# Optimization experiments

Measured on AMD Instinct MI355X. Metric: run time of the kernel, lower is better.

Reference implementation:

```python
import jax, jax.numpy as jnp
import numpy as np

N, E = 100000, 1600000
D_IN, D_HID, D_OUT = 128, 64, 64
NEG_SLOPE = 0.2


def setup_inputs() -> dict:
    key = jax.random.key(0)
    ks = jax.random.split(key, 12)
    x = jax.random.normal(ks[0], (N, D_IN), dtype=jnp.float32)
    edge_index = jax.random.randint(ks[1], (2, E), 0, N, dtype=jnp.int64)
    edge_attr = jax.random.normal(ks[2], (E, 8), dtype=jnp.float32)
    s1 = 1.0 / np.sqrt(D_IN)
    s2 = 1.0 / np.sqrt(D_HID)
    return {
        "x": x,
        "edge_index": edge_index,
        "edge_attr": edge_attr,
        "W1": jax.random.normal(ks[3], (D_IN, D_HID), dtype=jnp.float32) * s1,
        "att_src1": jax.random.normal(ks[4], (D_HID,), dtype=jnp.float32) * s2,
        "att_dst1": jax.random.normal(ks[5], (D_HID,), dtype=jnp.float32) * s2,
        "b1": jnp.zeros((D_HID,), dtype=jnp.float32),
        "W2": jax.random.normal(ks[6], (D_HID, D_OUT), dtype=jnp.float32) * s2,
        "att_src2": jax.random.normal(ks[7], (D_OUT,), dtype=jnp.float32) * (1.0 / np.sqrt(D_OUT)),
        "att_dst2": jax.random.normal(ks[8], (D_OUT,), dtype=jnp.float32) * (1.0 / np.sqrt(D_OUT)),
        "b2": jnp.zeros((D_OUT,), dtype=jnp.float32),
    }


def gat_conv(x, src, dst, W, att_src, att_dst, b, n_nodes):
    # h = W x  (single head)
    h = x @ W                                   # [N, F]
    a_src = h @ att_src                         # [N]
    a_dst = h @ att_dst                         # [N]
    e = jax.nn.leaky_relu(a_src[src] + a_dst[dst], NEG_SLOPE)  # [E]
    # softmax over incoming edges per target node (numerically stable)
    e_max = jax.ops.segment_max(e, dst, num_segments=n_nodes)
    w = jnp.exp(e - e_max[dst])
    denom = jax.ops.segment_sum(w, dst, num_segments=n_nodes)
    alpha = w / (denom[dst] + 1e-16)            # [E]
    out = jax.ops.segment_sum(h[src] * alpha[:, None], dst, num_segments=n_nodes)
    return out + b


def reference(x, edge_index, edge_attr, W1, att_src1, att_dst1, b1, W2, att_src2, att_dst2, b2):
    n_nodes = x.shape[0]
    # PyG GATConv default: add self-loops; edge_attr unused (edge_dim=None)
    loops = jnp.arange(n_nodes, dtype=edge_index.dtype)
    src = jnp.concatenate([edge_index[0], loops])
    dst = jnp.concatenate([edge_index[1], loops])
    h = gat_conv(x, src, dst, W1, att_src1, att_dst1, b1, n_nodes)
    h = jax.nn.relu(h)
    h = gat_conv(h, src, dst, W2, att_src2, att_dst2, b2, n_nodes)
    # global_mean_pool with batch=None -> mean over all nodes, shape [1, D_OUT]
    return jnp.mean(h, axis=0, keepdims=True)
```

## Files before the change

kernel.cpp:

```cpp
#include <hip/hip_runtime.h>
#include <hip/hip_bf16.h>
#include <cstdint>

#define NEG_SLOPE 0.2f
#define BUCKET_SHIFT 9
#define CHUNK 4096

typedef __attribute__((ext_vector_type(4))) int            i32x4;
typedef __attribute__((ext_vector_type(4))) float          f32x4;
typedef __attribute__((ext_vector_type(8))) unsigned short u16x8;
typedef __attribute__((ext_vector_type(4))) unsigned short u16x4;

__device__ inline unsigned short f2bf(float f) {
    unsigned xi = __float_as_uint(f);
    unsigned r = xi + 0x7fffu + ((xi >> 16) & 1u);
    return (unsigned short)(r >> 16);
}
__device__ inline float bflo(unsigned g) { return __uint_as_float(g << 16); }
__device__ inline float bfhi(unsigned g) { return __uint_as_float(g & 0xffff0000u); }

__device__ inline int get_ei(const int* ei, int is64, long idx) {
    return is64 ? ei[2 * idx] : ei[(int)idx];
}

__device__ inline int detect_is64(const int* __restrict__ ei, int tid) {
    __shared__ int dred[4];
    int v = 0;
    for (int i = tid; i < 2048; i += 256) v |= ei[2 * i + 1];
#pragma unroll
    for (int off = 32; off; off >>= 1) v |= __shfl_xor(v, off);
    if ((tid & 63) == 0) dred[tid >> 6] = v;
    __syncthreads();
    int r = dred[0] | dred[1] | dred[2] | dred[3];
    __syncthreads();
    return (r == 0) ? 1 : 0;
}

__device__ void p1_body(const int* __restrict__ ei, int* __restrict__ BT,
                        int E, int n, int bid) {
    __shared__ int cnt[256];
    int tid = threadIdx.x;
    int is64 = detect_is64(ei, tid);
    int nbuk = (n + 511) >> BUCKET_SHIFT;
    for (int b = tid; b < nbuk; b += 256) cnt[b] = 0;
    __syncthreads();
    int total = E + n;
    int beg = bid * CHUNK;
    int end = beg + CHUNK; if (end > total) end = total;
    for (int i = beg + tid; i < end; i += 256) {
        int d = (i < E) ? get_ei(ei, is64, (long)E + i) : (i - E);
        atomicAdd(&cnt[d >> BUCKET_SHIFT], 1);
    }
    __syncthreads();
    for (int b = tid; b < nbuk; b += 256)
        if (cnt[b]) atomicAdd(&BT[b], cnt[b]);
}

#define MFMA_BF16(acc, a, b) \
    asm("s_nop 1\n\tv_mfma_f32_16x16x32_bf16 %0, %1, %2, %0" \
        : "+v"(acc) : "v"(a), "v"(b))

template <int KT, bool XBF>
__device__ void proj_body(const void* __restrict__ xin,
                          const unsigned short* __restrict__ Wp,
                          const float* __restrict__ att_s,
                          const float* __restrict__ att_d,
                          unsigned short* __restrict__ h2,
                          float* __restrict__ asrc,
                          float* __restrict__ adst, int n, int bid) {
    constexpr int K = 32 * KT;
    __shared__ alignas(16) unsigned short lb[4][16 * 72];
    int tid = threadIdx.x;
    int wid = tid >> 6, l = tid & 63;
    int lm = l & 15, lg = l >> 4;

    int node0 = bid * 64 + wid * 16;
    if (node0 >= n) return;

    float as_c[4], ad_c[4];
#pragma unroll
    for (int ct = 0; ct < 4; ++ct) {
        as_c[ct] = att_s[16 * ct + lm];
        ad_c[ct] = att_d[16 * ct + lm];
    }

    f32x4 acc[4] = {};
    int arow = node0 + lm;
    bool rowok = arow < n;

#pragma unroll
    for (int kt = 0; kt < KT; ++kt) {
        i32x4 af = {0, 0, 0, 0};
        if (XBF) {
            const unsigned short* xb = (const unsigned short*)xin
                                       + (size_t)arow * K + 32 * kt + 8 * lg;
            if (rowok) af = *(const i32x4*)xb;
        } else {
            const float* xp = (const float*)xin + (size_t)arow * K + 8 * lg + 32 * kt;
            float4 v0 = make_float4(0.f, 0.f, 0.f, 0.f);
            float4 v1 = v0;
            if (rowok) {
                v0 = *(const float4*)(xp);
                v1 = *(const float4*)(xp + 4);
            }
            af[0] = (int)((unsigned)f2bf(v0.x) | ((unsigned)f2bf(v0.y) << 16));
            af[1] = (int)((unsigned)f2bf(v0.z) | ((unsigned)f2bf(v0.w) << 16));
            af[2] = (int)((unsigned)f2bf(v1.x) | ((unsigned)f2bf(v1.y) << 16));
            af[3] = (int)((unsigned)f2bf(v1.z) | ((unsigned)f2bf(v1.w) << 16));
        }
#pragma unroll
        for (int ct = 0; ct < 4; ++ct) {
            i32x4 bf = *(const i32x4*)(Wp + (((kt * 4 + ct) * 64) + l) * 8);
            MFMA_BF16(acc[ct], af, bf);
        }
    }
    asm volatile("s_nop 7\n\ts_nop 7"
                 : "+v"(acc[0]), "+v"(acc[1]), "+v"(acc[2]), "+v"(acc[3]));

    float ps[4], pd[4];
#pragma unroll
    for (int r = 0; r < 4; ++r) {
        float s = 0.f, d = 0.f;
#pragma unroll
        for (int ct = 0; ct < 4; ++ct) {
            s = fmaf(acc[ct][r], as_c[ct], s);
            d = fmaf(acc[ct][r], ad_c[ct], d);
        }
        ps[r] = s; pd[r] = d;
    }
#pragma unroll
    for (int off = 1; off < 16; off <<= 1) {
#pragma unroll
        for (int r = 0; r < 4; ++r) {
            ps[r] += __shfl_xor(ps[r], off);
            pd[r] += __shfl_xor(pd[r], off);
        }
    }
    if (lm == 0) {
#pragma unroll
        for (int r = 0; r < 4; ++r) {
            int node = node0 + 4 * lg + r;
            if (node < n) { asrc[node] = ps[r]; adst[node] = pd[r]; }
        }
    }

    unsigned short* wb = lb[wid];
#pragma unroll
    for (int ct = 0; ct < 4; ++ct)
#pragma unroll
        for (int r = 0; r < 4; ++r)
            wb[(4 * lg + r) * 72 + 16 * ct + lm] = f2bf(acc[ct][r]);
    asm volatile("s_waitcnt lgkmcnt(0)" ::: "memory");
    int ch = l & 7;
#pragma unroll
    for (int p = 0; p < 2; ++p) {
        int rr = (l >> 3) + 8 * p;
        u16x8 ov = *(const u16x8*)(wb + rr * 72 + 8 * ch);
        int onode = node0 + rr;
        if (onode < n)
            *(u16x8*)(h2 + (size_t)onode * 64 + 8 * ch) = ov;
    }
}

__global__ __launch_bounds__(256) void prep_kernel(const float* __restrict__ W1,
                                                   const float* __restrict__ W2,
                                                   unsigned short* __restrict__ wp1,
                                                   unsigned short* __restrict__ wp2,
                                                   int* __restrict__ BT, int nbuk) {
    if (blockIdx.x == 6) {
        for (int b = threadIdx.x; b < nbuk; b += 256) BT[b] = 0;
        return;
    }
    int t = blockIdx.x * 256 + threadIdx.x;
    int f = t >> 6, l = t & 63;
    int lm = l & 15, lg = l >> 4;
    const float* W = (f < 16) ? W1 : W2;
    unsigned short* wp = (f < 16) ? wp1 : wp2;
    int idx = (f < 16) ? f : (f - 16);
    int kt = idx >> 2, ct = idx & 3;
    union { u16x8 v; unsigned short u[8]; } o;
#pragma unroll
    for (int e = 0; e < 8; ++e)
        o.u[e] = f2bf(W[(size_t)(32 * kt + 8 * lg + e) * 64 + 16 * ct + lm]);
    *(u16x8*)(wp + ((size_t)idx * 64 + l) * 8) = o.v;
}

__global__ __launch_bounds__(256) void fused1(const float* __restrict__ x,
                                              const unsigned short* __restrict__ wp1,
                                              const float* __restrict__ as1,
                                              const float* __restrict__ ad1,
                                              unsigned short* __restrict__ h2,
                                              float* __restrict__ asrc,
                                              float* __restrict__ adst, int n,
                                              const int* __restrict__ ei,
                                              int* __restrict__ BT, int E, int pgrid) {
    if ((int)blockIdx.x < pgrid)
        proj_body<4, false>(x, wp1, as1, ad1, h2, asrc, adst, n, blockIdx.x);
    else
        p1_body(ei, BT, E, n, blockIdx.x - pgrid);
}

__global__ __launch_bounds__(256) void scan_bt(const int* __restrict__ BT,
                                               int* __restrict__ BB,
                                               int* __restrict__ cur, int nbuk) {
    __shared__ int s[256];
    int t = threadIdx.x;
    int v = (t < nbuk) ? BT[t] : 0;
    s[t] = v;
    __syncthreads();
    for (int off = 1; off < 256; off <<= 1) {
        int u = (t >= off) ? s[t - off] : 0;
        __syncthreads();
        s[t] += u;
        __syncthreads();
    }
    int exc = s[t] - v;
    if (t < nbuk) { BB[t] = exc; cur[t] = exc; }
    if (t == 0) BB[nbuk] = s[255];
}

__global__ __launch_bounds__(256) void p3_scatter(const int* __restrict__ ei,
                                                  int* __restrict__ cur,
                                                  int* __restrict__ sorted,
                                                  int E, int n) {
    __shared__ int stash[CHUNK];
    __shared__ unsigned char stashB[CHUNK];
    __shared__ int cnt[256];
    __shared__ int base[256];
    int tid = threadIdx.x;
    int is64 = detect_is64(ei, tid);
    int nbuk = (n + 511) >> BUCKET_SHIFT;
    for (int b = tid; b < nbuk; b += 256) cnt[b] = 0;
    __syncthreads();
    int total = E + n;
    int beg = blockIdx.x * CHUNK;
    int end = beg + CHUNK; if (end > total) end = total;
    for (int i = beg + tid; i < end; i += 256) {
        int s, d;
        if (i < E) {
            s = get_ei(ei, is64, i);
            d = get_ei(ei, is64, (long)E + i);
        } else {
            s = d = i - E;
        }
        int li = i - beg;
        stash[li] = (s << BUCKET_SHIFT) | (d & 511);
        stashB[li] = (unsigned char)(d >> BUCKET_SHIFT);
        atomicAdd(&cnt[d >> BUCKET_SHIFT], 1);
    }
    __syncthreads();
    for (int b = tid; b < nbuk; b += 256) {
        int c = cnt[b];
        base[b] = c ? atomicAdd(&cur[b], c) : 0;
        cnt[b] = 0;
    }
    __syncthreads();
    int cc = end - beg;
    for (int li = tid; li < cc; li += 256) {
        int b = stashB[li];
        int p = base[b] + atomicAdd(&cnt[b], 1);
        sorted[p] = stash[li];
    }
}

__global__ __launch_bounds__(256) void p4_finalize(const int* __restrict__ BB,
                                                   const int* __restrict__ sorted,
                                                   int* __restrict__ ptr,
                                                   int* __restrict__ csr_src,
                                                   int n, int T) {
    int b = blockIdx.x;
    int tid = threadIdx.x;
    int node0 = b << BUCKET_SHIFT;
    int nn = n - node0; if (nn > 512) nn = 512;
    int beg = BB[b];
    int end = BB[b + 1];

    __shared__ int cnt[512];
    __shared__ int pair[256];
    __shared__ int exc[512];
    cnt[tid] = 0; cnt[tid + 256] = 0;
    __syncthreads();
    for (int j = beg + tid; j < end; j += 256) {
        int v = sorted[j];
        atomicAdd(&cnt[v & 511], 1);
    }
    __syncthreads();
    int psum = cnt[2 * tid] + cnt[2 * tid + 1];
    pair[tid] = psum;
    __syncthreads();
    for (int off = 1; off < 256; off <<= 1) {
        int u = (tid >= off) ? pair[tid - off] : 0;
        __syncthreads();
        pair[tid] += u;
        __syncthreads();
    }
    int pexc = pair[tid] - psum;
    exc[2 * tid] = pexc;
    exc[2 * tid + 1] = pexc + cnt[2 * tid];
    __syncthreads();
    for (int i = tid; i < nn; i += 256) ptr[node0 + i] = beg + exc[i];
    if (node0 + nn == n && tid == 0) ptr[n] = T;
    cnt[tid] = exc[tid]; cnt[tid + 256] = exc[tid + 256];
    __syncthreads();
    for (int j = beg + tid; j < end; j += 256) {
        int v = sorted[j];
        int p = beg + atomicAdd(&cnt[v & 511], 1);
        csr_src[p] = ((unsigned)v) >> BUCKET_SHIFT;
    }
}

__global__ __launch_bounds__(256) void proj2_kernel(const unsigned short* __restrict__ xin,
                                                    const unsigned short* __restrict__ wp2,
                                                    const float* __restrict__ as2,
                                                    const float* __restrict__ ad2,
                                                    unsigned short* __restrict__ h2,
                                                    float* __restrict__ asrc,
                                                    float* __restrict__ adst, int n) {
    proj_body<2, true>(xin, wp2, as2, ad2, h2, asrc, adst, n, blockIdx.x);
}

template <bool FMEAN>
__global__ __launch_bounds__(256) void agg_kernel(const int* __restrict__ ptr,
                                                  const int* __restrict__ srcs,
                                                  const unsigned short* __restrict__ h2,
                                                  const float* __restrict__ asrc,
                                                  const float* __restrict__ adst,
                                                  const float* __restrict__ bias,
                                                  unsigned short* __restrict__ outbf,
                                                  float* __restrict__ partials,
                                                  int n, int do_relu) {
    __shared__ int2  sm[4][64];
    __shared__ float red[256];
    int tid = threadIdx.x;
    int lane = tid & 63, wid = tid >> 6;
    int slot = lane >> 4, f = lane & 15;
    const char* h2b = (const char*)h2;
    unsigned fo = (unsigned)f << 3;
    float4 bv = *(const float4*)(bias + 4 * f);
    float ms0 = 0.f, ms1 = 0.f, ms2 = 0.f, ms3 = 0.f;

    int gwave = (blockIdx.x * blockDim.x + tid) >> 6;
    int nwaves = (gridDim.x * blockDim.x) >> 6;
    for (int node = gwave; node < n; node += nwaves) {
        int beg = ptr[node], end = ptr[node + 1];
        float ad = adst[node];
        float a0 = 0.f, a1 = 0.f, a2 = 0.f, a3 = 0.f, wsum = 0.f;
        for (int b = beg; b < end; b += 64) {
            int blen = end - b; if (blen > 64) blen = 64;
            int sv = 0; float wv = 0.f;
            if (lane < blen) {
                sv = srcs[b + lane];
                float e = asrc[sv] + ad;
                e = (e > 0.f) ? e : NEG_SLOPE * e;
                wv = __expf(e);
            }
            wsum += wv;
            sm[wid][lane] = make_int2(sv, __float_as_int(wv));
            int ni = (blen + 15) >> 4;
            for (int j = 0; j < ni; ++j) {
                int2 swv[4];
#pragma unroll
                for (int u = 0; u < 4; ++u)
                    swv[u] = sm[wid][16 * j + 4 * u + slot];
                uint2 g[4]; float w[4];
#pragma unroll
                for (int u = 0; u < 4; ++u) {
                    w[u] = __int_as_float(swv[u].y);
                    g[u] = *(const uint2*)(h2b + (((unsigned)swv[u].x << 7) + fo));
                }
#pragma unroll
                for (int u = 0; u < 4; ++u) {
                    a0 = fmaf(w[u], bflo(g[u].x), a0);
                    a1 = fmaf(w[u], bfhi(g[u].x), a1);
                    a2 = fmaf(w[u], bflo(g[u].y), a2);
                    a3 = fmaf(w[u], bfhi(g[u].y), a3);
                }
            }
        }
        a0 += __shfl_xor(a0, 16); a0 += __shfl_xor(a0, 32);
        a1 += __shfl_xor(a1, 16); a1 += __shfl_xor(a1, 32);
        a2 += __shfl_xor(a2, 16); a2 += __shfl_xor(a2, 32);
        a3 += __shfl_xor(a3, 16); a3 += __shfl_xor(a3, 32);
#pragma unroll
        for (int off = 32; off; off >>= 1) wsum += __shfl_xor(wsum, off);
        float inv = 1.f / (wsum + 1e-16f);
        float o0 = a0 * inv + bv.x;
        float o1 = a1 * inv + bv.y;
        float o2 = a2 * inv + bv.z;
        float o3 = a3 * inv + bv.w;
        if (!FMEAN) {
            if (do_relu) {
                o0 = fmaxf(o0, 0.f); o1 = fmaxf(o1, 0.f);
                o2 = fmaxf(o2, 0.f); o3 = fmaxf(o3, 0.f);
            }
            if (slot == 0) {
                u16x4 ov;
                ov[0] = f2bf(o0); ov[1] = f2bf(o1);
                ov[2] = f2bf(o2); ov[3] = f2bf(o3);
                *(u16x4*)(outbf + (size_t)node * 64 + 4 * f) = ov;
            }
        } else {
            if (slot == 0) { ms0 += o0; ms1 += o1; ms2 += o2; ms3 += o3; }
        }
    }
    if (FMEAN) {
        if (slot == 0)
            *(float4*)(red + wid * 64 + 4 * f) = make_float4(ms0, ms1, ms2, ms3);
        __syncthreads();
        if (tid < 64) {
            float t = red[tid] + red[64 + tid] + red[128 + tid] + red[192 + tid];
            partials[(size_t)blockIdx.x * 64 + tid] = t;
        }
    }
}

__global__ __launch_bounds__(256) void reduce1(const float* __restrict__ partials,
                                               float* __restrict__ out256, int nb) {
    __shared__ float red[256];
    int f = threadIdx.x & 63;
    int w = threadIdx.x >> 6;
    float s = 0.f;
    for (int r = blockIdx.x + 256 * w; r < nb; r += 1024)
        s += partials[(size_t)r * 64 + f];
    red[threadIdx.x] = s;
    __syncthreads();
    if (w == 0) {
        float t = red[f] + red[64 + f] + red[128 + f] + red[192 + f];
        out256[(size_t)blockIdx.x * 64 + f] = t;
    }
}

__global__ __launch_bounds__(1024) void reduce2(const float* __restrict__ out256,
                                                float* __restrict__ out, float inv_n) {
    __shared__ float red[1024];
    int f = threadIdx.x & 63;
    int w = threadIdx.x >> 6;
    float s = 0.f;
    for (int r = w; r < 256; r += 16) s += out256[(size_t)r * 64 + f];
    red[threadIdx.x] = s;
    __syncthreads();
    for (int step = 8; step >= 1; step >>= 1) {
        if (w < step) red[w * 64 + f] += red[(w + step) * 64 + f];
        __syncthreads();
    }
    if (w == 0) out[f] = red[f] * inv_n;
}

extern "C" void kernel_launch(void* const* d_in, const int* in_sizes, int n_in,
                              void* d_out, int out_size, void* d_ws, size_t ws_size,
                              hipStream_t stream) {
    const float* x   = (const float*)d_in[0];
    const int*   ei  = (const int*)d_in[1];
    const float* W1  = (const float*)d_in[3];
    const float* as1 = (const float*)d_in[4];
    const float* ad1 = (const float*)d_in[5];
    const float* b1  = (const float*)d_in[6];
    const float* W2  = (const float*)d_in[7];
    const float* as2 = (const float*)d_in[8];
    const float* ad2 = (const float*)d_in[9];
    const float* b2  = (const float*)d_in[10];
    float* out = (float*)d_out;

    const int N = in_sizes[0] / 128;
    const int E = in_sizes[1] / 2;
    const int T = E + N;

    const int NBUK  = (N + 511) >> BUCKET_SHIFT;
    const int NBLK  = (T + CHUNK - 1) / CHUNK;
    const int PGRID = (N + 63) / 64;
    const int AGRID = (N + 3) / 4;

    size_t off = 0;
    char* base = (char*)d_ws;
    auto alloc = [&](size_t bytes) -> void* {
        void* p = base + off;
        off += (bytes + 255) & ~(size_t)255;
        return p;
    };
    int*   ptr     = (int*)alloc(((size_t)N + 1) * 4);
    int*   BT      = (int*)alloc(256 * 4);
    int*   BB      = (int*)alloc(257 * 4);
    int*   cur     = (int*)alloc(256 * 4);
    int*   csr_src = (int*)alloc((size_t)T * 4);
    float* asrc    = (float*)alloc((size_t)N * 4);
    float* adst    = (float*)alloc((size_t)N * 4);
    unsigned short* h2 = (unsigned short*)alloc((size_t)N * 64 * 2);
    unsigned short* bufB = (unsigned short*)alloc((size_t)N * 64 * 4);
    unsigned short* wp1 = (unsigned short*)alloc(16 * 64 * 8 * 2);
    unsigned short* wp2 = (unsigned short*)alloc(8 * 64 * 8 * 2);
    float* out256  = (float*)alloc(256 * 64 * 4);
    int*   sorted  = (int*)bufB;
    float* partials = (float*)bufB;
    (void)ws_size;

    prep_kernel<<<7, 256, 0, stream>>>(W1, W2, wp1, wp2, BT, NBUK);
    fused1<<<PGRID + NBLK, 256, 0, stream>>>(x, wp1, as1, ad1, h2, asrc, adst, N,
                                             ei, BT, E, PGRID);
    scan_bt<<<1, 256, 0, stream>>>(BT, BB, cur, NBUK);
    p3_scatter<<<NBLK, 256, 0, stream>>>(ei, cur, sorted, E, N);
    p4_finalize<<<NBUK, 256, 0, stream>>>(BB, sorted, ptr, csr_src, N, T);
    agg_kernel<false><<<AGRID, 256, 0, stream>>>(ptr, csr_src, h2, asrc, adst,
                                                 b1, bufB, nullptr, N, 1);
    proj2_kernel<<<PGRID, 256, 0, stream>>>(bufB, wp2, as2, ad2, h2, asrc, adst, N);
    agg_kernel<true><<<AGRID, 256, 0, stream>>>(ptr, csr_src, h2, asrc, adst,
                                                b2, nullptr, partials, N, 0);
    reduce1<<<256, 256, 0, stream>>>(partials, out256, AGRID);
    reduce2<<<1, 1024, 0, stream>>>(out256, out, 1.f / (float)N);
}
```

Measured before the change: 315.2 us.

## Assign one node per 16-lane group instead of per wavefront in aggregation

The aggregation kernel now gives each destination node to a 16-lane group, so one wavefront works on four nodes at once. Before, a whole 64-lane wave handled one node and split its edges across four slots. With an average in-degree of about 17, that left most lanes idle during edge-weight computation. Edges are now staged 16 at a time into a padded per-group shared buffer, each group reduces its weight sum with its own shuffles, and the cross-slot accumulator shuffles are gone. The grid shrinks to match. Nodes in the same wave now have different degrees, which adds divergence inside the wave.

```diff
diff --git a/kernel.cpp b/kernel.cpp
--- a/kernel.cpp
+++ b/kernel.cpp
@@ -329,39 +329,39 @@
                                                   unsigned short* __restrict__ outbf,
                                                   float* __restrict__ partials,
                                                   int n, int do_relu) {
-    __shared__ int2  sm[4][64];
-    __shared__ float red[256];
+    __shared__ int2  sm[4][4][17];
+    __shared__ float4 red4[256];
     int tid = threadIdx.x;
     int lane = tid & 63, wid = tid >> 6;
-    int slot = lane >> 4, f = lane & 15;
+    int grp = lane >> 4, f = lane & 15;
     const char* h2b = (const char*)h2;
     unsigned fo = (unsigned)f << 3;
     float4 bv = *(const float4*)(bias + 4 * f);
     float ms0 = 0.f, ms1 = 0.f, ms2 = 0.f, ms3 = 0.f;
 
-    int gwave = (blockIdx.x * blockDim.x + tid) >> 6;
-    int nwaves = (gridDim.x * blockDim.x) >> 6;
-    for (int node = gwave; node < n; node += nwaves) {
+    int gg = (blockIdx.x * blockDim.x + tid) >> 4;
+    int ng = (gridDim.x * blockDim.x) >> 4;
+    for (int node = gg; node < n; node += ng) {
         int beg = ptr[node], end = ptr[node + 1];
         float ad = adst[node];
         float a0 = 0.f, a1 = 0.f, a2 = 0.f, a3 = 0.f, wsum = 0.f;
-        for (int b = beg; b < end; b += 64) {
-            int blen = end - b; if (blen > 64) blen = 64;
+        for (int b = beg; b < end; b += 16) {
+            int blen = end - b; if (blen > 16) blen = 16;
             int sv = 0; float wv = 0.f;
-            if (lane < blen) {
-                sv = srcs[b + lane];
+            if (f < blen) {
+                sv = srcs[b + f];
                 float e = asrc[sv] + ad;
                 e = (e > 0.f) ? e : NEG_SLOPE * e;
                 wv = __expf(e);
             }
             wsum += wv;
-            sm[wid][lane] = make_int2(sv, __float_as_int(wv));
-            int ni = (blen + 15) >> 4;
+            sm[wid][grp][f] = make_int2(sv, __float_as_int(wv));
+            int ni = (blen + 3) >> 2;
             for (int j = 0; j < ni; ++j) {
                 int2 swv[4];
 #pragma unroll
                 for (int u = 0; u < 4; ++u)
-                    swv[u] = sm[wid][16 * j + 4 * u + slot];
+                    swv[u] = sm[wid][grp][4 * j + u];
                 uint2 g[4]; float w[4];
 #pragma unroll
                 for (int u = 0; u < 4; ++u) {
@@ -377,12 +377,10 @@
                 }
             }
         }
-        a0 += __shfl_xor(a0, 16); a0 += __shfl_xor(a0, 32);
-        a1 += __shfl_xor(a1, 16); a1 += __shfl_xor(a1, 32);
-        a2 += __shfl_xor(a2, 16); a2 += __shfl_xor(a2, 32);
-        a3 += __shfl_xor(a3, 16); a3 += __shfl_xor(a3, 32);
-#pragma unroll
-        for (int off = 32; off; off >>= 1) wsum += __shfl_xor(wsum, off);
+        wsum += __shfl_xor(wsum, 1);
+        wsum += __shfl_xor(wsum, 2);
+        wsum += __shfl_xor(wsum, 4);
+        wsum += __shfl_xor(wsum, 8);
         float inv = 1.f / (wsum + 1e-16f);
         float o0 = a0 * inv + bv.x;
         float o1 = a1 * inv + bv.y;
@@ -393,23 +391,25 @@
                 o0 = fmaxf(o0, 0.f); o1 = fmaxf(o1, 0.f);
                 o2 = fmaxf(o2, 0.f); o3 = fmaxf(o3, 0.f);
             }
-            if (slot == 0) {
-                u16x4 ov;
-                ov[0] = f2bf(o0); ov[1] = f2bf(o1);
-                ov[2] = f2bf(o2); ov[3] = f2bf(o3);
-                *(u16x4*)(outbf + (size_t)node * 64 + 4 * f) = ov;
+            u16x4 ov;
+            ov[0] = f2bf(o0); ov[1] = f2bf(o1);
+            ov[2] = f2bf(o2); ov[3] = f2bf(o3);
+            *(u16x4*)(outbf + (size_t)node * 64 + 4 * f) = ov;
+        } else {
+            ms0 += o0; ms1 += o1; ms2 += o2; ms3 += o3;
+        }
+    }
+    if (FMEAN) {
+        red4[tid] = make_float4(ms0, ms1, ms2, ms3);
+        __syncthreads();
+        if (tid < 16) {
+            float4 s = make_float4(0.f, 0.f, 0.f, 0.f);
+#pragma unroll
+            for (int r = 0; r < 16; ++r) {
+                float4 v = red4[r * 16 + tid];
+                s.x += v.x; s.y += v.y; s.z += v.z; s.w += v.w;
             }
-        } else {
-            if (slot == 0) { ms0 += o0; ms1 += o1; ms2 += o2; ms3 += o3; }
-        }
-    }
-    if (FMEAN) {
-        if (slot == 0)
-            *(float4*)(red + wid * 64 + 4 * f) = make_float4(ms0, ms1, ms2, ms3);
-        __syncthreads();
-        if (tid < 64) {
-            float t = red[tid] + red[64 + tid] + red[128 + tid] + red[192 + tid];
-            partials[(size_t)blockIdx.x * 64 + tid] = t;
+            *(float4*)(partials + (size_t)blockIdx.x * 64 + 4 * tid) = s;
         }
     }
 }
@@ -468,7 +468,7 @@
     const int NBUK  = (N + 511) >> BUCKET_SHIFT;
     const int NBLK  = (T + CHUNK - 1) / CHUNK;
     const int PGRID = (N + 63) / 64;
-    const int AGRID = (N + 3) / 4;
+    const int AGRID = (N + 15) / 16;
 
     size_t off = 0;
     char* base = (char*)d_ws;
```

Result: faster. 293.8 us (-6.8%).
